# Kernel tuning notes

Measured on AMD Instinct MI355X. Metric: run time of the kernel, lower is better.

The kernel has to match this reference:

```python
import jax, jax.numpy as jnp
import numpy as np

S, B = 64, 16          # seq_len, batch
V = 32000              # ntoken
NINP = 512             # ninp (embedding / decoder input dim)
NHID = 1536            # nhid (intermediate LSTM layers)
NHL = 1024             # nhidlast (last LSTM layer)
E = 8                  # n_experts


def setup_inputs() -> dict:
    key = jax.random.key(0)
    ks = jax.random.split(key, 24)

    def unif(k, shape, r=0.1):
        return jax.random.uniform(k, shape, jnp.float32, -r, r)

    inp = {
        "tokens": jax.random.randint(ks[0], (S, B), 0, V),
        "h0": jnp.zeros((B, NHID), jnp.float32),
        "c0": jnp.zeros((B, NHID), jnp.float32),
        "h1": jnp.zeros((B, NHID), jnp.float32),
        "c1": jnp.zeros((B, NHID), jnp.float32),
        "h2": jnp.zeros((B, NHL), jnp.float32),
        "c2": jnp.zeros((B, NHL), jnp.float32),
        # parameters
        "emb": unif(ks[1], (V, NINP)),
        "Wih0": unif(ks[2], (4 * NHID, NINP)),
        "Whh0": unif(ks[3], (4 * NHID, NHID)),
        "b0": jnp.zeros((4 * NHID,), jnp.float32),
        "Wih1": unif(ks[4], (4 * NHID, NHID)),
        "Whh1": unif(ks[5], (4 * NHID, NHID)),
        "b1": jnp.zeros((4 * NHID,), jnp.float32),
        "Wih2": unif(ks[6], (4 * NHL, NHID)),
        "Whh2": unif(ks[7], (4 * NHL, NHL)),
        "b2": jnp.zeros((4 * NHL,), jnp.float32),
        "prior_W": unif(ks[8], (E, NHL)),
        "latent_W": unif(ks[9], (E * NINP, NHL)),
        "latent_b": jnp.zeros((E * NINP,), jnp.float32),
        "dec_W": unif(ks[10], (V, NINP)),
        "dec_b": jnp.zeros((V,), jnp.float32),
        "gain": jnp.ones((NINP,), jnp.float32),   # decoder_gain (frozen ones)
    }
    return inp


def _lstm_layer(x, h0, c0, Wih, Whh, b):
    # x: (S, B, Din); gate order i, f, g, o as in torch
    xg = jnp.einsum('sbd,gd->sbg', x, Wih) + b  # precompute input projections

    def step(carry, xt):
        h, c = carry
        g = xt + h @ Whh.T
        i, f, gg, o = jnp.split(g, 4, axis=-1)
        c = jax.nn.sigmoid(f) * c + jax.nn.sigmoid(i) * jnp.tanh(gg)
        h = jax.nn.sigmoid(o) * jnp.tanh(c)
        return (h, c), h

    (hT, cT), ys = jax.lax.scan(step, (h0, c0), xg)
    return ys, hT, cT


def reference(tokens, h0, c0, h1, c1, h2, c2, emb, Wih0, Whh0, b0,
              Wih1, Whh1, b1, Wih2, Whh2, b2, prior_W, latent_W, latent_b,
              dec_W, dec_b, gain):
    x = emb[tokens]                                   # (S, B, NINP)
    x, _, _ = _lstm_layer(x, h0, c0, Wih0, Whh0, b0)  # (S, B, NHID)
    x, _, _ = _lstm_layer(x, h1, c1, Wih1, Whh1, b1)  # (S, B, NHID)
    out, _, _ = _lstm_layer(x, h2, c2, Wih2, Whh2, b2)  # (S, B, NHL)

    # MoS head
    latent = jnp.tanh(jnp.einsum('sbh,eh->sbe', out, latent_W) + latent_b)
    latent = latent.reshape(S * B * E, NINP)          # (S*B*E, NINP)
    logit = (latent * gain) @ dec_W.T + dec_b         # (S*B*E, V)
    prior = jax.nn.softmax(out.reshape(S * B, NHL) @ prior_W.T, axis=-1)  # (S*B, E)
    prob = jax.nn.softmax(logit, axis=-1).reshape(S * B, E, V)
    prob = jnp.einsum('nev,ne->nv', prob, prior)      # mixture over experts
    log_prob = jnp.log(prob + 1e-8)
    return log_prob.reshape(S, B, V)
```

## Files before the change

### kernel.cpp

```cpp
#include <hip/hip_runtime.h>
#include <hip/hip_bf16.h>

typedef __attribute__((ext_vector_type(8))) short short8;
typedef __attribute__((ext_vector_type(4))) float f32x4;
typedef unsigned short u16;
typedef unsigned long long u64;

__device__ __forceinline__ u16 f2b(float f) {
    unsigned u = __float_as_uint(f);
    return (u16)((u + 0x7FFFu + ((u >> 16) & 1u)) >> 16);
}
__device__ __forceinline__ float b2f(u16 u) {
    return __uint_as_float(((unsigned)u) << 16);
}
__device__ __forceinline__ void gload16(const void* g, void* l) {
    __builtin_amdgcn_global_load_lds(
        (const __attribute__((address_space(1))) void*)g,
        (__attribute__((address_space(3))) void*)l, 16, 0, 0);
}

struct CvtJobs {
    const float* s[6];
    u16* d[6];
    int n4[6];
    int njobs;
};

__global__ __launch_bounds__(256)
void k_f2b(const float* __restrict__ s, u16* __restrict__ d, int n4)
{
    int i = blockIdx.x * 256 + threadIdx.x;
    if (i >= n4) return;
    float4 v = ((const float4*)s)[i];
    short4 o;
    o.x = (short)f2b(v.x); o.y = (short)f2b(v.y);
    o.z = (short)f2b(v.z); o.w = (short)f2b(v.w);
    ((short4*)d)[i] = o;
}

__global__ __launch_bounds__(256)
void k_embed(const int* __restrict__ tok, const float* __restrict__ emb,
             u16* __restrict__ x0)
{
    int i = blockIdx.x * 256 + threadIdx.x;
    int n = i >> 7, p4 = i & 127;
    float4 v = ((const float4*)(emb + (size_t)tok[n] * 512))[p4];
    short4 o;
    o.x = (short)f2b(v.x); o.y = (short)f2b(v.y);
    o.z = (short)f2b(v.z); o.w = (short)f2b(v.w);
    ((short4*)x0)[i] = o;
}

template <int EPI>
__global__ __launch_bounds__(256)
void k_gemm(const u16* __restrict__ A, const u16* __restrict__ B,
            const float* __restrict__ bias, void* __restrict__ Cp,
            int M, int N, int K, const float* __restrict__ gain,
            float* __restrict__ rsum)
{
    __shared__ __align__(16) u16 As[2][128 * 32];
    __shared__ __align__(16) u16 Bs[2][128 * 32];
    __shared__ float rs[2][128];
    const int tid = threadIdx.x;
    const int lane = tid & 63, wid = tid >> 6;
    const int wr = wid >> 1, wc = wid & 1;
    const int l15 = lane & 15, l4 = lane >> 4;
    const int row0 = blockIdx.y * 128, col0 = blockIdx.x * 128;

    const int srA = wid * 16 + (lane >> 2);
    const int skA = (lane & 3) * 8;

    auto stage = [&](int buf, int k0) {
        gload16(A + (size_t)(row0 + srA) * K + k0 + skA, &As[buf][wid * 512]);
        gload16(A + (size_t)(row0 + 64 + srA) * K + k0 + skA, &As[buf][2048 + wid * 512]);
        gload16(B + (size_t)(col0 + srA) * K + k0 + skA, &Bs[buf][wid * 512]);
        gload16(B + (size_t)(col0 + 64 + srA) * K + k0 + skA, &Bs[buf][2048 + wid * 512]);
    };

    f32x4 acc[4][4] = {};

    stage(0, 0);
    __syncthreads();
    int cur = 0;
    for (int k0 = 0; k0 < K; k0 += 32) {
        if (k0 + 32 < K) stage(cur ^ 1, k0 + 32);

        short8 af[4], bfv[4];
#pragma unroll
        for (int i = 0; i < 4; ++i)
            af[i]  = *(const short8*)&As[cur][(wr * 64 + i * 16 + l15) * 32 + l4 * 8];
#pragma unroll
        for (int i = 0; i < 4; ++i)
            bfv[i] = *(const short8*)&Bs[cur][(wc * 64 + i * 16 + l15) * 32 + l4 * 8];
#pragma unroll
        for (int mi = 0; mi < 4; ++mi)
#pragma unroll
            for (int ni = 0; ni < 4; ++ni)
                acc[mi][ni] = __builtin_amdgcn_mfma_f32_16x16x32_bf16(
                    af[mi], bfv[ni], acc[mi][ni], 0, 0, 0);
        __syncthreads();
        cur ^= 1;
    }

    if (EPI == 2) {
#pragma unroll
        for (int mi = 0; mi < 4; ++mi) {
#pragma unroll
            for (int j = 0; j < 4; ++j) {
                int rb = row0 + wr * 64 + mi * 16 + l4 * 4 + j;
                float rsub = 0.f;
#pragma unroll
                for (int ni = 0; ni < 4; ++ni) {
                    int cc = col0 + wc * 64 + ni * 16 + l15;
                    float pv = expf(fminf(acc[mi][ni][j] + bias[cc], 80.f));
                    ((u16*)Cp)[(size_t)rb * N + cc] = f2b(pv);
                    rsub += pv;
                }
#pragma unroll
                for (int o = 1; o < 16; o <<= 1) rsub += __shfl_xor(rsub, o, 64);
                if (l15 == 0)
                    rs[wc][wr * 64 + mi * 16 + l4 * 4 + j] = rsub;
            }
        }
        __syncthreads();
        if (tid < 128)
            atomicAdd(&rsum[row0 + tid], rs[0][tid] + rs[1][tid]);
        return;
    }

#pragma unroll
    for (int mi = 0; mi < 4; ++mi) {
#pragma unroll
        for (int ni = 0; ni < 4; ++ni) {
            int rb = row0 + wr * 64 + mi * 16 + l4 * 4;
            int cc = col0 + wc * 64 + ni * 16 + l15;
            float bv = bias[cc];
#pragma unroll
            for (int j = 0; j < 4; ++j) {
                float v = acc[mi][ni][j] + bv;
                if (EPI == 0) {
                    ((float*)Cp)[(size_t)(rb + j) * N + cc] = v;
                } else {
                    int e = cc >> 9, pp = cc & 511;
                    ((u16*)Cp)[(((size_t)(rb + j) * 8 + e) << 9) | pp] =
                        f2b(tanhf(v) * gain[pp]);
                }
            }
        }
    }
}

__global__ __launch_bounds__(512)
void k_gemm_dec(const u16* __restrict__ A, const u16* __restrict__ B,
                const float* __restrict__ bias, u16* __restrict__ pe,
                int M, int N, int K, float* __restrict__ rsum,
                const u16* __restrict__ pePrev, const float* __restrict__ prior,
                const float* __restrict__ rsumPrev, float* __restrict__ outp,
                int n0prev, int nPer)
{
    __shared__ __align__(16) u16 As[2][256 * 32];
    __shared__ __align__(16) u16 Bs[2][128 * 32];
    __shared__ float rs[2][256];
    const int tid = threadIdx.x;

    if ((int)blockIdx.y == (int)gridDim.y - 1) {
        if (n0prev < 0) return;
        float* wsh = (float*)As;
        for (int i = tid; i < nPer * 8; i += 512)
            wsh[i] = prior[(size_t)(n0prev + (i >> 3)) * 8 + (i & 7)]
                   / rsumPrev[i];
        __syncthreads();
        const int total = nPer * 32000;
        const int stride = gridDim.x * 512;
        for (int i = blockIdx.x * 512 + tid; i < total; i += stride) {
            int nl = i / 32000, v = i - nl * 32000;
            float acc = 0.f;
#pragma unroll
            for (int e = 0; e < 8; ++e)
                acc += b2f(pePrev[(size_t)(nl * 8 + e) * 32000 + v])
                     * wsh[nl * 8 + e];
            outp[(size_t)(n0prev + nl) * 32000 + v] = logf(acc + 1e-8f);
        }
        return;
    }

    const int lane = tid & 63, wid = tid >> 6;
    const int wr = wid >> 1, wc = wid & 1;
    const int l15 = lane & 15, l4 = lane >> 4;
    const int row0 = blockIdx.y * 256, col0 = blockIdx.x * 128;

    const int srA = wid * 16 + (lane >> 2);
    const int skA = (lane & 3) * 8;

    auto stage = [&](int buf, int k0) {
        gload16(A + (size_t)(row0 + srA) * K + k0 + skA, &As[buf][wid * 512]);
        gload16(A + (size_t)(row0 + 128 + srA) * K + k0 + skA, &As[buf][4096 + wid * 512]);
        gload16(B + (size_t)(col0 + srA) * K + k0 + skA, &Bs[buf][wid * 512]);
    };

    f32x4 acc[4][4] = {};

    stage(0, 0);
    __syncthreads();
    int cur = 0;
    for (int k0 = 0; k0 < K; k0 += 32) {
        if (k0 + 32 < K) stage(cur ^ 1, k0 + 32);

        short8 af[4], bfv[4];
#pragma unroll
        for (int i = 0; i < 4; ++i)
            af[i]  = *(const short8*)&As[cur][(wr * 64 + i * 16 + l15) * 32 + l4 * 8];
#pragma unroll
        for (int i = 0; i < 4; ++i)
            bfv[i] = *(const short8*)&Bs[cur][(wc * 64 + i * 16 + l15) * 32 + l4 * 8];
#pragma unroll
        for (int mi = 0; mi < 4; ++mi)
#pragma unroll
            for (int ni = 0; ni < 4; ++ni)
                acc[mi][ni] = __builtin_amdgcn_mfma_f32_16x16x32_bf16(
                    af[mi], bfv[ni], acc[mi][ni], 0, 0, 0);
        __syncthreads();
        cur ^= 1;
    }

#pragma unroll
    for (int mi = 0; mi < 4; ++mi) {
#pragma unroll
        for (int j = 0; j < 4; ++j) {
            int rloc = wr * 64 + mi * 16 + l4 * 4 + j;
            float rsub = 0.f;
#pragma unroll
            for (int ni = 0; ni < 4; ++ni) {
                int cc = col0 + wc * 64 + ni * 16 + l15;
                float pv = expf(fminf(acc[mi][ni][j] + bias[cc], 80.f));
                pe[(size_t)(row0 + rloc) * N + cc] = f2b(pv);
                rsub += pv;
            }
#pragma unroll
            for (int o = 1; o < 16; o <<= 1) rsub += __shfl_xor(rsub, o, 64);
            if (l15 == 0) rs[wc][rloc] = rsub;
        }
    }
    __syncthreads();
    if (tid < 256)
        atomicAdd(&rsum[row0 + tid], rs[0][tid] + rs[1][tid]);
}

template <int DH>
__global__ void __launch_bounds__(512)
k_rnn(const float* __restrict__ xg,
      const u16* __restrict__ W,
      const float* __restrict__ h0f,
      const float* __restrict__ c0f,
      u16* __restrict__ y,
      unsigned* __restrict__ bar,
      int nb, CvtJobs jobs)
{
    if ((int)blockIdx.x >= nb) {
        const int hb = blockIdx.x - nb, nh = gridDim.x - nb;
        for (int j = 0; j < jobs.njobs; ++j) {
            const float4* s = (const float4*)jobs.s[j];
            short4* d = (short4*)jobs.d[j];
            const int n4 = jobs.n4[j];
            for (int i = hb * 512 + threadIdx.x; i < n4; i += nh * 512) {
                float4 v = s[i];
                short4 o;
                o.x = (short)f2b(v.x); o.y = (short)f2b(v.y);
                o.z = (short)f2b(v.z); o.w = (short)f2b(v.w);
                d[i] = o;
            }
        }
        return;
    }

    constexpr int DH2 = DH / 2;
    constexpr int NSH = DH2 / 32;
    constexpr int NL  = 16 * DH / 4 / 512;
    constexpr int RW  = DH / 4;
    constexpr int LDH = DH + 8;
    __shared__ __align__(16) u16 hs[16][LDH];
    __shared__ __align__(16) f32x4 red[8][64];
    __shared__ __align__(16) u16 hout[16][16];

    const int tid = threadIdx.x;
    const int lane = tid & 63, wid = tid >> 6;
    const int g = wid & 3, kh = wid >> 2;
    const int l15 = lane & 15, l4 = lane >> 4;
    const int u0 = blockIdx.x * 16;

    short8 wfr[NSH];
    {
        const u16* wa = W + (size_t)(g * DH + u0 + l15) * DH + kh * DH2 + l4 * 8;
#pragma unroll
        for (int s = 0; s < NSH; ++s) wfr[s] = *(const short8*)(wa + s * 32);
    }

    const int eb = tid >> 4, eu = tid & 15;
    float c_reg = (tid < 256) ? c0f[(size_t)eb * DH + u0 + eu] : 0.f;

    for (int t = 0; t < 64; ++t) {
        float xpre[4];
        if (tid < 256) {
            const float* xr = xg + (size_t)(t * 16 + eb) * 4 * DH + u0 + eu;
#pragma unroll
            for (int gg = 0; gg < 4; ++gg) xpre[gg] = xr[(size_t)gg * DH];
        }

        if (t == 0) {
            for (int i = tid; i < 16 * DH / 4; i += 512) {
                int r = i / (DH / 4), k4 = i % (DH / 4);
                float4 v = *(const float4*)(h0f + (size_t)r * DH + k4 * 4);
                short4 o;
                o.x = (short)f2b(v.x); o.y = (short)f2b(v.y);
                o.z = (short)f2b(v.z); o.w = (short)f2b(v.w);
                *(short4*)&hs[r][k4 * 4] = o;
            }
            __syncthreads();
        } else {
            if (tid < nb) {
                while (__hip_atomic_load(bar + tid * 32, __ATOMIC_RELAXED,
                                         __HIP_MEMORY_SCOPE_AGENT) < (unsigned)t)
                    __builtin_amdgcn_s_sleep(1);
            }
            __syncthreads();
            const u64* hp = (const u64*)(y + (size_t)(t - 1) * 16 * DH);
            u64 tmp[NL];
#pragma unroll
            for (int j = 0; j < NL; ++j)
                tmp[j] = __hip_atomic_load(hp + tid + j * 512, __ATOMIC_RELAXED,
                                           __HIP_MEMORY_SCOPE_AGENT);
#pragma unroll
            for (int j = 0; j < NL; ++j) {
                int idx = tid + j * 512;
                int r = idx / RW, c = (idx % RW) * 4;
                *(u64*)&hs[r][c] = tmp[j];
            }
            __syncthreads();
        }

        f32x4 acc = {};
#pragma unroll
        for (int s = 0; s < NSH; ++s) {
            short8 hf = *(const short8*)&hs[l15][kh * DH2 + s * 32 + l4 * 8];
            acc = __builtin_amdgcn_mfma_f32_16x16x32_bf16(hf, wfr[s], acc, 0, 0, 0);
        }
        red[wid][lane] = acc;
        __syncthreads();

        if (tid < 256) {
            const int li = (eb >> 2) * 16 + eu, j = eb & 3;
            float gt[4];
#pragma unroll
            for (int gg = 0; gg < 4; ++gg)
                gt[gg] = ((const float*)&red[gg][li])[j]
                       + ((const float*)&red[4 + gg][li])[j]
                       + xpre[gg];
            float si = 1.f / (1.f + expf(-gt[0]));
            float sf = 1.f / (1.f + expf(-gt[1]));
            float so = 1.f / (1.f + expf(-gt[3]));
            c_reg = sf * c_reg + si * tanhf(gt[2]);
            hout[eb][eu] = f2b(so * tanhf(c_reg));
        }
        __syncthreads();

        if (tid < 64) {
            int r = tid >> 2, c4 = (tid & 3) * 4;
            u64 v = *(const u64*)&hout[r][c4];
            __hip_atomic_store((u64*)(y + (size_t)(t * 16 + r) * DH + u0 + c4), v,
                               __ATOMIC_RELAXED, __HIP_MEMORY_SCOPE_AGENT);
        }

        if (t < 63) {
            __syncthreads();
            if (tid == 0)
                __hip_atomic_store(bar + blockIdx.x * 32, (unsigned)(t + 1),
                                   __ATOMIC_RELAXED, __HIP_MEMORY_SCOPE_AGENT);
        }
    }
}

__global__ __launch_bounds__(256)
void k_prior(const u16* __restrict__ out2, const float* __restrict__ pW,
             float* __restrict__ prior)
{
    const int n = blockIdx.x;
    const int tid = threadIdx.x;
    const int e = tid >> 5, lane = tid & 31;
    const u16* x = out2 + (size_t)n * 1024;
    const float* w = pW + (size_t)e * 1024;
    float s = 0.f;
    for (int k = lane; k < 1024; k += 32) s += b2f(x[k]) * w[k];
#pragma unroll
    for (int o = 16; o; o >>= 1) s += __shfl_down(s, o, 32);
    __shared__ float es[8];
    if (lane == 0) es[e] = s;
    __syncthreads();
    if (tid == 0) {
        float m = -1e30f;
        for (int i = 0; i < 8; ++i) m = fmaxf(m, es[i]);
        float Z = 0.f, ex[8];
        for (int i = 0; i < 8; ++i) { ex[i] = expf(es[i] - m); Z += ex[i]; }
        for (int i = 0; i < 8; ++i) prior[(size_t)n * 8 + i] = ex[i] / Z;
    }
}

__global__ __launch_bounds__(128)
void k_combine(const u16* __restrict__ pe, const float* __restrict__ prior,
               const float* __restrict__ rsum, float* __restrict__ out, int n0)
{
    const int v2 = blockIdx.x * 128 + threadIdx.x;
    const int nl = blockIdx.y;
    __shared__ float w[8];
    if (threadIdx.x < 8)
        w[threadIdx.x] = prior[(size_t)(n0 + nl) * 8 + threadIdx.x]
                       / rsum[nl * 8 + threadIdx.x];
    __syncthreads();
    float a0 = 0.f, a1 = 0.f;
#pragma unroll
    for (int e = 0; e < 8; ++e) {
        unsigned pv = *(const unsigned*)&pe[(size_t)(nl * 8 + e) * 32000 + v2 * 2];
        a0 += b2f((u16)(pv & 0xffff)) * w[e];
        a1 += b2f((u16)(pv >> 16)) * w[e];
    }
    float2 o;
    o.x = logf(a0 + 1e-8f);
    o.y = logf(a1 + 1e-8f);
    *(float2*)&out[(size_t)(n0 + nl) * 32000 + v2 * 2] = o;
}

extern "C" void kernel_launch(void* const* d_in, const int* in_sizes, int n_in,
                              void* d_out, int out_size, void* d_ws, size_t ws_size,
                              hipStream_t stream)
{
    const int*   tok  = (const int*)d_in[0];
    const float* h0   = (const float*)d_in[1];
    const float* c0   = (const float*)d_in[2];
    const float* h1   = (const float*)d_in[3];
    const float* c1   = (const float*)d_in[4];
    const float* h2   = (const float*)d_in[5];
    const float* c2   = (const float*)d_in[6];
    const float* emb  = (const float*)d_in[7];
    const float* Wih0 = (const float*)d_in[8];
    const float* Whh0 = (const float*)d_in[9];
    const float* b0   = (const float*)d_in[10];
    const float* Wih1 = (const float*)d_in[11];
    const float* Whh1 = (const float*)d_in[12];
    const float* b1   = (const float*)d_in[13];
    const float* Wih2 = (const float*)d_in[14];
    const float* Whh2 = (const float*)d_in[15];
    const float* b2   = (const float*)d_in[16];
    const float* priW = (const float*)d_in[17];
    const float* latW = (const float*)d_in[18];
    const float* latb = (const float*)d_in[19];
    const float* decW = (const float*)d_in[20];
    const float* decb = (const float*)d_in[21];
    const float* gain = (const float*)d_in[22];

    char* p = (char*)d_ws;
    auto alloc = [&](size_t bytes) {
        char* r = p; p += (bytes + 255) & ~(size_t)255; return r;
    };
    u16* Whh0b = (u16*)alloc(6144ull * 1536 * 2);
    u16* Whh1b = (u16*)alloc(6144ull * 1536 * 2);
    u16* Whh2b = (u16*)alloc(4096ull * 1024 * 2);
    u16* latWb = (u16*)alloc(4096ull * 1024 * 2);
    u16* decWb = (u16*)alloc(32000ull * 512 * 2);
    u16* latb16 = (u16*)alloc(8192ull * 512 * 2);
    float* pri   = (float*)alloc(8192 * 4);
    float* rowsum = (float*)alloc(8192 * 4);
    u16* out2 = (u16*)alloc(1024ull * 1024 * 2);
    unsigned* bars = (unsigned*)alloc(3 * 96 * 32 * 4);
    char* trans = p;
    u16* Wih0b = (u16*)alloc(6144ull * 512 * 2);
    u16* Wih1b = (u16*)alloc(6144ull * 1536 * 2);
    u16* Wih2b = (u16*)alloc(4096ull * 1536 * 2);
    u16* x0 = (u16*)alloc(1024ull * 512 * 2);
    u16* x1 = (u16*)alloc(1024ull * 1536 * 2);
    u16* x2 = (u16*)alloc(1024ull * 1536 * 2);
    float* xg = (float*)alloc(1024ull * 6144 * 4);
    size_t cap = ws_size - (size_t)(trans - (char*)d_ws);
    int chunkRows;
    bool fused;
    if      (cap >= 2ull * 1024 * 32000 * 2) { chunkRows = 1024; fused = true; }
    else if (cap >= 2ull * 512 * 32000 * 2)  { chunkRows = 512;  fused = true; }
    else if (cap >= 2ull * 256 * 32000 * 2)  { chunkRows = 256;  fused = true; }
    else                                     { chunkRows = 128;  fused = false; }
    int nPer = chunkRows / 8;
    size_t chunkElems = (size_t)chunkRows * 32000;
    u16* pe0 = (u16*)trans;
    u16* pe1 = pe0 + chunkElems;

    hipMemsetAsync(bars, 0, 3 * 96 * 32 * 4, stream);
    hipMemsetAsync(rowsum, 0, 8192 * 4, stream);

    k_f2b<<<9216, 256, 0, stream>>>(Whh0, Whh0b, 2359296);
    k_f2b<<<3072, 256, 0, stream>>>(Wih0, Wih0b, 786432);
    k_embed<<<512, 256, 0, stream>>>(tok, emb, x0);

    k_gemm<0><<<dim3(48, 8), 256, 0, stream>>>(
        x0, Wih0b, b0, xg, 1024, 6144, 512, nullptr, nullptr);
    {
        unsigned* bar = bars;
        int nb = 96;
        CvtJobs jobs;
        jobs.s[0] = Whh1; jobs.d[0] = Whh1b; jobs.n4[0] = 2359296;
        jobs.s[1] = Whh2; jobs.d[1] = Whh2b; jobs.n4[1] = 1048576;
        jobs.s[2] = Wih1; jobs.d[2] = Wih1b; jobs.n4[2] = 2359296;
        jobs.s[3] = Wih2; jobs.d[3] = Wih2b; jobs.n4[3] = 1572864;
        jobs.s[4] = latW; jobs.d[4] = latWb; jobs.n4[4] = 1048576;
        jobs.s[5] = decW; jobs.d[5] = decWb; jobs.n4[5] = 4096000;
        jobs.njobs = 6;
        void* args[] = {(void*)&xg, (void*)&Whh0b, (void*)&h0, (void*)&c0,
                        (void*)&x1, (void*)&bar, (void*)&nb, (void*)&jobs};
        hipLaunchCooperativeKernel(reinterpret_cast<void*>(&k_rnn<1536>),
                                   dim3(256), dim3(512), args, 0, stream);
    }

    k_gemm<0><<<dim3(48, 8), 256, 0, stream>>>(
        x1, Wih1b, b1, xg, 1024, 6144, 1536, nullptr, nullptr);
    {
        unsigned* bar = bars + 96 * 32;
        int nb = 96;
        CvtJobs jobs;
        jobs.njobs = 0;
        void* args[] = {(void*)&xg, (void*)&Whh1b, (void*)&h1, (void*)&c1,
                        (void*)&x2, (void*)&bar, (void*)&nb, (void*)&jobs};
        hipLaunchCooperativeKernel(reinterpret_cast<void*>(&k_rnn<1536>),
                                   dim3(96), dim3(512), args, 0, stream);
    }

    k_gemm<0><<<dim3(32, 8), 256, 0, stream>>>(
        x2, Wih2b, b2, xg, 1024, 4096, 1536, nullptr, nullptr);
    {
        unsigned* bar = bars + 2 * 96 * 32;
        int nb = 64;
        CvtJobs jobs;
        jobs.njobs = 0;
        void* args[] = {(void*)&xg, (void*)&Whh2b, (void*)&h2, (void*)&c2,
                        (void*)&out2, (void*)&bar, (void*)&nb, (void*)&jobs};
        hipLaunchCooperativeKernel(reinterpret_cast<void*>(&k_rnn<1024>),
                                   dim3(64), dim3(512), args, 0, stream);
    }

    k_prior<<<1024, 256, 0, stream>>>(out2, priW, pri);
    k_gemm<1><<<dim3(32, 8), 256, 0, stream>>>(
        out2, latWb, latb, latb16, 1024, 4096, 1024, gain, nullptr);

    if (fused) {
        const int rowTiles = chunkRows / 256;
        const int nChunks = 1024 / nPer;
        for (int ci = 0; ci < nChunks; ++ci) {
            int nb = ci * nPer;
            u16* peCur = (ci & 1) ? pe1 : pe0;
            const u16* pePrev = (ci & 1) ? pe0 : pe1;
            int n0prev = nb - nPer;
            const float* rsPrev = rowsum + (size_t)(n0prev < 0 ? 0 : n0prev) * 8;
            k_gemm_dec<<<dim3(250, rowTiles + 1), 512, 0, stream>>>(
                latb16 + (size_t)nb * 8 * 512, decWb, decb, peCur,
                chunkRows, 32000, 512, rowsum + (size_t)nb * 8,
                pePrev, pri, rsPrev, (float*)d_out, n0prev, nPer);
        }
        int n0t = 1024 - nPer;
        const u16* peLast = ((nChunks - 1) & 1) ? pe1 : pe0;
        k_combine<<<dim3(125, nPer), 128, 0, stream>>>(
            peLast, pri, rowsum + (size_t)n0t * 8, (float*)d_out, n0t);
    } else {
        for (int nb = 0; nb < 1024; nb += nPer) {
            const u16* Ach = latb16 + (size_t)nb * 8 * 512;
            float* rsumc = rowsum + (size_t)nb * 8;
            k_gemm<2><<<dim3(250, chunkRows / 128), 256, 0, stream>>>(
                Ach, decWb, decb, pe0, chunkRows, 32000, 512, nullptr, rsumc);
            k_combine<<<dim3(125, nPer), 128, 0, stream>>>(
                pe0, pri, rsumc, (float*)d_out, nb);
        }
    }
}
```

Measured before the change: 1.424 ms.

## Replace per-step flag barrier with sentinel-polled hidden state in recurrent kernel

Drops the per-block step-counter barrier in the persistent LSTM kernel. Output buffers are now pre-filled with 0xFF, and each thread polls its own 8-byte chunk of the previous hidden state until it no longer holds the all-ones sentinel. This removes one barrier round trip per timestep, both the flag store and the polling load, and lets threads proceed as soon as their data arrives. The cost is three extra memsets, plus a reliance on no valid bf16 quad ever equalling the all-ones pattern (a NaN pattern) and on the 8-byte stores being atomic.

```diff
diff --git a/kernel.cpp b/kernel.cpp
--- a/kernel.cpp
+++ b/kernel.cpp
@@ -5,6 +5,8 @@
 typedef __attribute__((ext_vector_type(4))) float f32x4;
 typedef unsigned short u16;
 typedef unsigned long long u64;
+
+#define SENT 0xFFFFFFFFFFFFFFFFull
 
 __device__ __forceinline__ u16 f2b(float f) {
     unsigned u = __float_as_uint(f);
@@ -253,7 +255,6 @@
       const float* __restrict__ h0f,
       const float* __restrict__ c0f,
       u16* __restrict__ y,
-      unsigned* __restrict__ bar,
       int nb, CvtJobs jobs)
 {
     if ((int)blockIdx.x >= nb) {
@@ -317,18 +318,25 @@
             }
             __syncthreads();
         } else {
-            if (tid < nb) {
-                while (__hip_atomic_load(bar + tid * 32, __ATOMIC_RELAXED,
-                                         __HIP_MEMORY_SCOPE_AGENT) < (unsigned)t)
-                    __builtin_amdgcn_s_sleep(1);
-            }
-            __syncthreads();
             const u64* hp = (const u64*)(y + (size_t)(t - 1) * 16 * DH);
             u64 tmp[NL];
 #pragma unroll
             for (int j = 0; j < NL; ++j)
                 tmp[j] = __hip_atomic_load(hp + tid + j * 512, __ATOMIC_RELAXED,
                                            __HIP_MEMORY_SCOPE_AGENT);
+            for (;;) {
+                bool done = true;
+#pragma unroll
+                for (int j = 0; j < NL; ++j) done &= (tmp[j] != SENT);
+                if (done) break;
+                __builtin_amdgcn_s_sleep(1);
+#pragma unroll
+                for (int j = 0; j < NL; ++j)
+                    if (tmp[j] == SENT)
+                        tmp[j] = __hip_atomic_load(hp + tid + j * 512,
+                                                   __ATOMIC_RELAXED,
+                                                   __HIP_MEMORY_SCOPE_AGENT);
+            }
 #pragma unroll
             for (int j = 0; j < NL; ++j) {
                 int idx = tid + j * 512;
@@ -369,13 +377,7 @@
             __hip_atomic_store((u64*)(y + (size_t)(t * 16 + r) * DH + u0 + c4), v,
                                __ATOMIC_RELAXED, __HIP_MEMORY_SCOPE_AGENT);
         }
-
-        if (t < 63) {
-            __syncthreads();
-            if (tid == 0)
-                __hip_atomic_store(bar + blockIdx.x * 32, (unsigned)(t + 1),
-                                   __ATOMIC_RELAXED, __HIP_MEMORY_SCOPE_AGENT);
-        }
+        if (t < 63) __syncthreads();
     }
 }
 
@@ -469,7 +471,6 @@
     float* pri   = (float*)alloc(8192 * 4);
     float* rowsum = (float*)alloc(8192 * 4);
     u16* out2 = (u16*)alloc(1024ull * 1024 * 2);
-    unsigned* bars = (unsigned*)alloc(3 * 96 * 32 * 4);
     char* trans = p;
     u16* Wih0b = (u16*)alloc(6144ull * 512 * 2);
     u16* Wih1b = (u16*)alloc(6144ull * 1536 * 2);
@@ -490,8 +491,10 @@
     u16* pe0 = (u16*)trans;
     u16* pe1 = pe0 + chunkElems;
 
-    hipMemsetAsync(bars, 0, 3 * 96 * 32 * 4, stream);
     hipMemsetAsync(rowsum, 0, 8192 * 4, stream);
+    hipMemsetAsync(x1, 0xFF, 1024ull * 1536 * 2, stream);
+    hipMemsetAsync(x2, 0xFF, 1024ull * 1536 * 2, stream);
+    hipMemsetAsync(out2, 0xFF, 1024ull * 1024 * 2, stream);
 
     k_f2b<<<9216, 256, 0, stream>>>(Whh0, Whh0b, 2359296);
     k_f2b<<<3072, 256, 0, stream>>>(Wih0, Wih0b, 786432);
@@ -500,7 +503,6 @@
     k_gemm<0><<<dim3(48, 8), 256, 0, stream>>>(
         x0, Wih0b, b0, xg, 1024, 6144, 512, nullptr, nullptr);
     {
-        unsigned* bar = bars;
         int nb = 96;
         CvtJobs jobs;
         jobs.s[0] = Whh1; jobs.d[0] = Whh1b; jobs.n4[0] = 2359296;
@@ -511,7 +513,7 @@
         jobs.s[5] = decW; jobs.d[5] = decWb; jobs.n4[5] = 4096000;
         jobs.njobs = 6;
         void* args[] = {(void*)&xg, (void*)&Whh0b, (void*)&h0, (void*)&c0,
-                        (void*)&x1, (void*)&bar, (void*)&nb, (void*)&jobs};
+                        (void*)&x1, (void*)&nb, (void*)&jobs};
         hipLaunchCooperativeKernel(reinterpret_cast<void*>(&k_rnn<1536>),
                                    dim3(256), dim3(512), args, 0, stream);
     }
@@ -519,12 +521,11 @@
     k_gemm<0><<<dim3(48, 8), 256, 0, stream>>>(
         x1, Wih1b, b1, xg, 1024, 6144, 1536, nullptr, nullptr);
     {
-        unsigned* bar = bars + 96 * 32;
         int nb = 96;
         CvtJobs jobs;
         jobs.njobs = 0;
         void* args[] = {(void*)&xg, (void*)&Whh1b, (void*)&h1, (void*)&c1,
-                        (void*)&x2, (void*)&bar, (void*)&nb, (void*)&jobs};
+                        (void*)&x2, (void*)&nb, (void*)&jobs};
         hipLaunchCooperativeKernel(reinterpret_cast<void*>(&k_rnn<1536>),
                                    dim3(96), dim3(512), args, 0, stream);
     }
@@ -532,12 +533,11 @@
     k_gemm<0><<<dim3(32, 8), 256, 0, stream>>>(
         x2, Wih2b, b2, xg, 1024, 4096, 1536, nullptr, nullptr);
     {
-        unsigned* bar = bars + 2 * 96 * 32;
         int nb = 64;
         CvtJobs jobs;
         jobs.njobs = 0;
         void* args[] = {(void*)&xg, (void*)&Whh2b, (void*)&h2, (void*)&c2,
-                        (void*)&out2, (void*)&bar, (void*)&nb, (void*)&jobs};
+                        (void*)&out2, (void*)&nb, (void*)&jobs};
         hipLaunchCooperativeKernel(reinterpret_cast<void*>(&k_rnn<1024>),
                                    dim3(64), dim3(512), args, 0, stream);
     }
```

After: 1.494 ms. 1.05x slower.

## Overlap next layer's input projection with recurrent steps via helper blocks

Applied to the files above, without the earlier changes.

Spare blocks in the cooperative RNN launch now compute the next LSTM layer's input-projection GEMM, reading fp32 weights and converting them on the fly. They poll per-block step flags, and each 128-row tile starts once its 8 timesteps of hidden output are published. This removes the separate Wih1/Wih2 conversions and the standalone projection GEMMs between layers. Double-buffered xg arrays (xgA/xgB) make this possible. In exchange, helper blocks compete with the latency-critical recurrent blocks for bandwidth, and they rely on relaxed atomics and spin-waiting, so visibility of the published hidden states depends on those flags.

```diff
diff --git a/kernel.cpp b/kernel.cpp
--- a/kernel.cpp
+++ b/kernel.cpp
@@ -19,11 +19,15 @@
         (__attribute__((address_space(3))) void*)l, 16, 0, 0);
 }
 
-struct CvtJobs {
-    const float* s[6];
-    u16* d[6];
-    int n4[6];
-    int njobs;
+struct HelperWork {
+    const float* cs[4]; u16* cd[4]; int cn4[4]; int ncvt;
+    const u16* ysrc;
+    const float* Wf;
+    const float* bias;
+    float* xgOut;
+    int K, NC4;
+    unsigned* flags; int nflags;
+    int doproj;
 };
 
 __global__ __launch_bounds__(256)
@@ -246,6 +250,81 @@
         atomicAdd(&rsum[row0 + tid], rs[0][tid] + rs[1][tid]);
 }
 
+__device__ void helper_proj(u16* lds, const HelperWork& hw, int hb, int nh)
+{
+    u16* As = lds;
+    u16* Bs = lds + 4096;
+    const int tid = threadIdx.x;
+    const int lane = tid & 63, wid = tid >> 6;
+    const int wr = wid >> 2, wc = wid & 3;
+    const int l15 = lane & 15, l4 = lane >> 4;
+    const int K = hw.K, NC4 = hw.NC4;
+    const int NC = NC4 >> 7, NT = 8 * NC;
+
+    for (int idx = hb; idx < NT; idx += nh) {
+        const int rg = idx / NC, ct = idx - rg * NC;
+        const int row0 = rg * 128, col0 = ct * 128;
+        if (tid < hw.nflags) {
+            const unsigned tgt = 8u * rg + 8u;
+            while (__hip_atomic_load(hw.flags + tid * 32, __ATOMIC_RELAXED,
+                                     __HIP_MEMORY_SCOPE_AGENT) < tgt)
+                __builtin_amdgcn_s_sleep(1);
+        }
+        __syncthreads();
+
+        f32x4 acc[4][2] = {};
+        for (int k0 = 0; k0 < K; k0 += 32) {
+#pragma unroll
+            for (int it = 0; it < 2; ++it) {
+                int i = tid + it * 512;
+                int r = i >> 3, c8 = i & 7;
+                u64 v = __hip_atomic_load(
+                    (const u64*)(hw.ysrc + (size_t)(row0 + r) * K + k0 + c8 * 4),
+                    __ATOMIC_RELAXED, __HIP_MEMORY_SCOPE_AGENT);
+                *(u64*)&As[r * 32 + c8 * 4] = v;
+            }
+            {
+                int srow = tid >> 2, q = tid & 3;
+                const float4* src =
+                    (const float4*)(hw.Wf + (size_t)(col0 + srow) * K + k0 + q * 8);
+                float4 v0 = src[0], v1 = src[1];
+                short8 o;
+                o[0] = (short)f2b(v0.x); o[1] = (short)f2b(v0.y);
+                o[2] = (short)f2b(v0.z); o[3] = (short)f2b(v0.w);
+                o[4] = (short)f2b(v1.x); o[5] = (short)f2b(v1.y);
+                o[6] = (short)f2b(v1.z); o[7] = (short)f2b(v1.w);
+                *(short8*)&Bs[srow * 32 + q * 8] = o;
+            }
+            __syncthreads();
+            short8 af[4], bfv[2];
+#pragma unroll
+            for (int i = 0; i < 4; ++i)
+                af[i] = *(const short8*)&As[(wr * 64 + i * 16 + l15) * 32 + l4 * 8];
+#pragma unroll
+            for (int i = 0; i < 2; ++i)
+                bfv[i] = *(const short8*)&Bs[(wc * 32 + i * 16 + l15) * 32 + l4 * 8];
+#pragma unroll
+            for (int mi = 0; mi < 4; ++mi)
+#pragma unroll
+                for (int ni = 0; ni < 2; ++ni)
+                    acc[mi][ni] = __builtin_amdgcn_mfma_f32_16x16x32_bf16(
+                        af[mi], bfv[ni], acc[mi][ni], 0, 0, 0);
+            __syncthreads();
+        }
+#pragma unroll
+        for (int mi = 0; mi < 4; ++mi)
+#pragma unroll
+            for (int ni = 0; ni < 2; ++ni) {
+                int rb = row0 + wr * 64 + mi * 16 + l4 * 4;
+                int cc = col0 + wc * 32 + ni * 16 + l15;
+                float bv = hw.bias[cc];
+#pragma unroll
+                for (int j = 0; j < 4; ++j)
+                    hw.xgOut[(size_t)(rb + j) * NC4 + cc] = acc[mi][ni][j] + bv;
+            }
+    }
+}
+
 template <int DH>
 __global__ void __launch_bounds__(512)
 k_rnn(const float* __restrict__ xg,
@@ -254,25 +333,8 @@
       const float* __restrict__ c0f,
       u16* __restrict__ y,
       unsigned* __restrict__ bar,
-      int nb, CvtJobs jobs)
-{
-    if ((int)blockIdx.x >= nb) {
-        const int hb = blockIdx.x - nb, nh = gridDim.x - nb;
-        for (int j = 0; j < jobs.njobs; ++j) {
-            const float4* s = (const float4*)jobs.s[j];
-            short4* d = (short4*)jobs.d[j];
-            const int n4 = jobs.n4[j];
-            for (int i = hb * 512 + threadIdx.x; i < n4; i += nh * 512) {
-                float4 v = s[i];
-                short4 o;
-                o.x = (short)f2b(v.x); o.y = (short)f2b(v.y);
-                o.z = (short)f2b(v.z); o.w = (short)f2b(v.w);
-                d[i] = o;
-            }
-        }
-        return;
-    }
-
+      int nb, HelperWork hw)
+{
     constexpr int DH2 = DH / 2;
     constexpr int NSH = DH2 / 32;
     constexpr int NL  = 16 * DH / 4 / 512;
@@ -283,6 +345,25 @@
     __shared__ __align__(16) u16 hout[16][16];
 
     const int tid = threadIdx.x;
+
+    if ((int)blockIdx.x >= nb) {
+        const int hb = blockIdx.x - nb, nh = gridDim.x - nb;
+        for (int j = 0; j < hw.ncvt; ++j) {
+            const float4* s = (const float4*)hw.cs[j];
+            short4* d = (short4*)hw.cd[j];
+            const int n4 = hw.cn4[j];
+            for (int i = hb * 512 + tid; i < n4; i += nh * 512) {
+                float4 v = s[i];
+                short4 o;
+                o.x = (short)f2b(v.x); o.y = (short)f2b(v.y);
+                o.z = (short)f2b(v.z); o.w = (short)f2b(v.w);
+                d[i] = o;
+            }
+        }
+        if (hw.doproj) helper_proj(&hs[0][0], hw, hb, nh);
+        return;
+    }
+
     const int lane = tid & 63, wid = tid >> 6;
     const int g = wid & 3, kh = wid >> 2;
     const int l15 = lane & 15, l4 = lane >> 4;
@@ -370,12 +451,10 @@
                                __ATOMIC_RELAXED, __HIP_MEMORY_SCOPE_AGENT);
         }
 
-        if (t < 63) {
-            __syncthreads();
-            if (tid == 0)
-                __hip_atomic_store(bar + blockIdx.x * 32, (unsigned)(t + 1),
-                                   __ATOMIC_RELAXED, __HIP_MEMORY_SCOPE_AGENT);
-        }
+        __syncthreads();
+        if (tid == 0)
+            __hip_atomic_store(bar + blockIdx.x * 32, (unsigned)(t + 1),
+                               __ATOMIC_RELAXED, __HIP_MEMORY_SCOPE_AGENT);
     }
 }
 
@@ -472,12 +551,11 @@
     unsigned* bars = (unsigned*)alloc(3 * 96 * 32 * 4);
     char* trans = p;
     u16* Wih0b = (u16*)alloc(6144ull * 512 * 2);
-    u16* Wih1b = (u16*)alloc(6144ull * 1536 * 2);
-    u16* Wih2b = (u16*)alloc(4096ull * 1536 * 2);
     u16* x0 = (u16*)alloc(1024ull * 512 * 2);
     u16* x1 = (u16*)alloc(1024ull * 1536 * 2);
     u16* x2 = (u16*)alloc(1024ull * 1536 * 2);
-    float* xg = (float*)alloc(1024ull * 6144 * 4);
+    float* xgA = (float*)alloc(1024ull * 6144 * 4);
+    float* xgB = (float*)alloc(1024ull * 6144 * 4);
     size_t cap = ws_size - (size_t)(trans - (char*)d_ws);
     int chunkRows;
     bool fused;
@@ -498,46 +576,47 @@
     k_embed<<<512, 256, 0, stream>>>(tok, emb, x0);
 
     k_gemm<0><<<dim3(48, 8), 256, 0, stream>>>(
-        x0, Wih0b, b0, xg, 1024, 6144, 512, nullptr, nullptr);
+        x0, Wih0b, b0, xgA, 1024, 6144, 512, nullptr, nullptr);
+
     {
         unsigned* bar = bars;
         int nb = 96;
-        CvtJobs jobs;
-        jobs.s[0] = Whh1; jobs.d[0] = Whh1b; jobs.n4[0] = 2359296;
-        jobs.s[1] = Whh2; jobs.d[1] = Whh2b; jobs.n4[1] = 1048576;
-        jobs.s[2] = Wih1; jobs.d[2] = Wih1b; jobs.n4[2] = 2359296;
-        jobs.s[3] = Wih2; jobs.d[3] = Wih2b; jobs.n4[3] = 1572864;
-        jobs.s[4] = latW; jobs.d[4] = latWb; jobs.n4[4] = 1048576;
-        jobs.s[5] = decW; jobs.d[5] = decWb; jobs.n4[5] = 4096000;
-        jobs.njobs = 6;
-        void* args[] = {(void*)&xg, (void*)&Whh0b, (void*)&h0, (void*)&c0,
-                        (void*)&x1, (void*)&bar, (void*)&nb, (void*)&jobs};
+        HelperWork hw;
+        hw.cs[0] = Whh1; hw.cd[0] = Whh1b; hw.cn4[0] = 2359296;
+        hw.cs[1] = Whh2; hw.cd[1] = Whh2b; hw.cn4[1] = 1048576;
+        hw.cs[2] = latW; hw.cd[2] = latWb; hw.cn4[2] = 1048576;
+        hw.cs[3] = decW; hw.cd[3] = decWb; hw.cn4[3] = 4096000;
+        hw.ncvt = 4;
+        hw.ysrc = x1; hw.Wf = Wih1; hw.bias = b1; hw.xgOut = xgB;
+        hw.K = 1536; hw.NC4 = 6144;
+        hw.flags = bars; hw.nflags = 96; hw.doproj = 1;
+        void* args[] = {(void*)&xgA, (void*)&Whh0b, (void*)&h0, (void*)&c0,
+                        (void*)&x1, (void*)&bar, (void*)&nb, (void*)&hw};
         hipLaunchCooperativeKernel(reinterpret_cast<void*>(&k_rnn<1536>),
                                    dim3(256), dim3(512), args, 0, stream);
     }
 
-    k_gemm<0><<<dim3(48, 8), 256, 0, stream>>>(
-        x1, Wih1b, b1, xg, 1024, 6144, 1536, nullptr, nullptr);
     {
         unsigned* bar = bars + 96 * 32;
         int nb = 96;
-        CvtJobs jobs;
-        jobs.njobs = 0;
-        void* args[] = {(void*)&xg, (void*)&Whh1b, (void*)&h1, (void*)&c1,
-                        (void*)&x2, (void*)&bar, (void*)&nb, (void*)&jobs};
+        HelperWork hw;
+        hw.ncvt = 0;
+        hw.ysrc = x2; hw.Wf = Wih2; hw.bias = b2; hw.xgOut = xgA;
+        hw.K = 1536; hw.NC4 = 4096;
+        hw.flags = bars + 96 * 32; hw.nflags = 96; hw.doproj = 1;
+        void* args[] = {(void*)&xgB, (void*)&Whh1b, (void*)&h1, (void*)&c1,
+                        (void*)&x2, (void*)&bar, (void*)&nb, (void*)&hw};
         hipLaunchCooperativeKernel(reinterpret_cast<void*>(&k_rnn<1536>),
-                                   dim3(96), dim3(512), args, 0, stream);
-    }
-
-    k_gemm<0><<<dim3(32, 8), 256, 0, stream>>>(
-        x2, Wih2b, b2, xg, 1024, 4096, 1536, nullptr, nullptr);
+                                   dim3(256), dim3(512), args, 0, stream);
+    }
+
     {
         unsigned* bar = bars + 2 * 96 * 32;
         int nb = 64;
-        CvtJobs jobs;
-        jobs.njobs = 0;
-        void* args[] = {(void*)&xg, (void*)&Whh2b, (void*)&h2, (void*)&c2,
-                        (void*)&out2, (void*)&bar, (void*)&nb, (void*)&jobs};
+        HelperWork hw;
+        hw.ncvt = 0; hw.doproj = 0;
+        void* args[] = {(void*)&xgA, (void*)&Whh2b, (void*)&h2, (void*)&c2,
+                        (void*)&out2, (void*)&bar, (void*)&nb, (void*)&hw};
         hipLaunchCooperativeKernel(reinterpret_cast<void*>(&k_rnn<1024>),
                                    dim3(64), dim3(512), args, 0, stream);
     }
```

Result: slower. 1.466 ms (+3.0%).

## Fuse weight conversion and prior into GEMMs, remap decoder tiles by XCD

Applied to the files above, without the earlier changes.

The first input-projection GEMM now reads fp32 Wih0 directly and converts it to bf16 while staging into LDS. An extra row of blocks converts Whh0 in parallel, which removes two standalone conversion launches and the Wih0b buffer. The prior softmax is folded into extra blocks of the latent GEMM, so k_prior is no longer a separate launch. The decoder GEMM block indices are remapped so that consecutive work items land on the same XCD for better L2 locality. The cost is per-tile conversion work inside the first GEMM and a serialized 32-row loop in the prior helper blocks.

```diff
diff --git a/kernel.cpp b/kernel.cpp
--- a/kernel.cpp
+++ b/kernel.cpp
@@ -25,18 +25,6 @@
     int n4[6];
     int njobs;
 };
-
-__global__ __launch_bounds__(256)
-void k_f2b(const float* __restrict__ s, u16* __restrict__ d, int n4)
-{
-    int i = blockIdx.x * 256 + threadIdx.x;
-    if (i >= n4) return;
-    float4 v = ((const float4*)s)[i];
-    short4 o;
-    o.x = (short)f2b(v.x); o.y = (short)f2b(v.y);
-    o.z = (short)f2b(v.z); o.w = (short)f2b(v.w);
-    ((short4*)d)[i] = o;
-}
 
 __global__ __launch_bounds__(256)
 void k_embed(const int* __restrict__ tok, const float* __restrict__ emb,
@@ -51,17 +39,58 @@
     ((short4*)x0)[i] = o;
 }
 
-template <int EPI>
+template <int EPI, int BIN, int HELP>
 __global__ __launch_bounds__(256)
-void k_gemm(const u16* __restrict__ A, const u16* __restrict__ B,
+void k_gemm(const u16* __restrict__ A, const void* __restrict__ Bp,
             const float* __restrict__ bias, void* __restrict__ Cp,
             int M, int N, int K, const float* __restrict__ gain,
-            float* __restrict__ rsum)
+            float* __restrict__ rsum,
+            const float* __restrict__ xs, void* __restrict__ xd, int xn)
 {
     __shared__ __align__(16) u16 As[2][128 * 32];
     __shared__ __align__(16) u16 Bs[2][128 * 32];
     __shared__ float rs[2][128];
     const int tid = threadIdx.x;
+
+    if (HELP == 1 && (int)blockIdx.y == (int)gridDim.y - 1) {
+        const float4* s = (const float4*)xs;
+        short4* d = (short4*)xd;
+        for (int i = blockIdx.x * 256 + tid; i < xn; i += gridDim.x * 256) {
+            float4 v = s[i];
+            short4 o;
+            o.x = (short)f2b(v.x); o.y = (short)f2b(v.y);
+            o.z = (short)f2b(v.z); o.w = (short)f2b(v.w);
+            d[i] = o;
+        }
+        return;
+    }
+    if (HELP == 2 && (int)blockIdx.y == (int)gridDim.y - 1) {
+        const float* pW = xs;
+        float* pri = (float*)xd;
+        const int e = tid >> 5, lane = tid & 31;
+        float* es = rs[0];
+        for (int ni = 0; ni < 32; ++ni) {
+            int n = blockIdx.x * 32 + ni;
+            const u16* x = A + (size_t)n * 1024;
+            const float* w = pW + (size_t)e * 1024;
+            float s = 0.f;
+            for (int k = lane; k < 1024; k += 32) s += b2f(x[k]) * w[k];
+#pragma unroll
+            for (int o = 16; o; o >>= 1) s += __shfl_down(s, o, 32);
+            if (lane == 0) es[e] = s;
+            __syncthreads();
+            if (tid == 0) {
+                float m = -1e30f;
+                for (int i = 0; i < 8; ++i) m = fmaxf(m, es[i]);
+                float Z = 0.f, ex[8];
+                for (int i = 0; i < 8; ++i) { ex[i] = expf(es[i] - m); Z += ex[i]; }
+                for (int i = 0; i < 8; ++i) pri[(size_t)n * 8 + i] = ex[i] / Z;
+            }
+            __syncthreads();
+        }
+        return;
+    }
+
     const int lane = tid & 63, wid = tid >> 6;
     const int wr = wid >> 1, wc = wid & 1;
     const int l15 = lane & 15, l4 = lane >> 4;
@@ -69,12 +98,31 @@
 
     const int srA = wid * 16 + (lane >> 2);
     const int skA = (lane & 3) * 8;
+    const int srow = tid >> 1, skh = (tid & 1) << 4;
 
     auto stage = [&](int buf, int k0) {
         gload16(A + (size_t)(row0 + srA) * K + k0 + skA, &As[buf][wid * 512]);
         gload16(A + (size_t)(row0 + 64 + srA) * K + k0 + skA, &As[buf][2048 + wid * 512]);
-        gload16(B + (size_t)(col0 + srA) * K + k0 + skA, &Bs[buf][wid * 512]);
-        gload16(B + (size_t)(col0 + 64 + srA) * K + k0 + skA, &Bs[buf][2048 + wid * 512]);
+        if (BIN == 1) {
+            const u16* B = (const u16*)Bp;
+            gload16(B + (size_t)(col0 + srA) * K + k0 + skA, &Bs[buf][wid * 512]);
+            gload16(B + (size_t)(col0 + 64 + srA) * K + k0 + skA, &Bs[buf][2048 + wid * 512]);
+        } else {
+            const float* Bf = (const float*)Bp;
+            const float4* sb = (const float4*)(Bf + (size_t)(col0 + srow) * K + k0 + skh);
+            float4 v0 = sb[0], v1 = sb[1], v2 = sb[2], v3 = sb[3];
+            short8 o0, o1;
+            o0[0] = (short)f2b(v0.x); o0[1] = (short)f2b(v0.y);
+            o0[2] = (short)f2b(v0.z); o0[3] = (short)f2b(v0.w);
+            o0[4] = (short)f2b(v1.x); o0[5] = (short)f2b(v1.y);
+            o0[6] = (short)f2b(v1.z); o0[7] = (short)f2b(v1.w);
+            o1[0] = (short)f2b(v2.x); o1[1] = (short)f2b(v2.y);
+            o1[2] = (short)f2b(v2.z); o1[3] = (short)f2b(v2.w);
+            o1[4] = (short)f2b(v3.x); o1[5] = (short)f2b(v3.y);
+            o1[6] = (short)f2b(v3.z); o1[7] = (short)f2b(v3.w);
+            *(short8*)&Bs[buf][srow * 32 + skh]     = o0;
+            *(short8*)&Bs[buf][srow * 32 + skh + 8] = o1;
+        }
     };
 
     f32x4 acc[4][4] = {};
@@ -163,16 +211,25 @@
     __shared__ float rs[2][256];
     const int tid = threadIdx.x;
 
-    if ((int)blockIdx.y == (int)gridDim.y - 1) {
+    const int gx = gridDim.x, gy = gridDim.y;
+    const int total = gx * gy;
+    const int f = (int)blockIdx.y * gx + (int)blockIdx.x;
+    const int q = total >> 3, r = total & 7;
+    const int xcd = f & 7, idx = f >> 3;
+    const int work = (xcd < r) ? xcd * (q + 1) + idx
+                               : r * (q + 1) + (xcd - r) * q + idx;
+    const int wx = work / gy, wy = work - wx * gy;
+
+    if (wy == gy - 1) {
         if (n0prev < 0) return;
         float* wsh = (float*)As;
         for (int i = tid; i < nPer * 8; i += 512)
             wsh[i] = prior[(size_t)(n0prev + (i >> 3)) * 8 + (i & 7)]
                    / rsumPrev[i];
         __syncthreads();
-        const int total = nPer * 32000;
-        const int stride = gridDim.x * 512;
-        for (int i = blockIdx.x * 512 + tid; i < total; i += stride) {
+        const int total2 = nPer * 32000;
+        const int stride = gx * 512;
+        for (int i = wx * 512 + tid; i < total2; i += stride) {
             int nl = i / 32000, v = i - nl * 32000;
             float acc = 0.f;
 #pragma unroll
@@ -187,7 +244,7 @@
     const int lane = tid & 63, wid = tid >> 6;
     const int wr = wid >> 1, wc = wid & 1;
     const int l15 = lane & 15, l4 = lane >> 4;
-    const int row0 = blockIdx.y * 256, col0 = blockIdx.x * 128;
+    const int row0 = wy * 256, col0 = wx * 128;
 
     const int srA = wid * 16 + (lane >> 2);
     const int skA = (lane & 3) * 8;
@@ -376,31 +433,6 @@
                 __hip_atomic_store(bar + blockIdx.x * 32, (unsigned)(t + 1),
                                    __ATOMIC_RELAXED, __HIP_MEMORY_SCOPE_AGENT);
         }
-    }
-}
-
-__global__ __launch_bounds__(256)
-void k_prior(const u16* __restrict__ out2, const float* __restrict__ pW,
-             float* __restrict__ prior)
-{
-    const int n = blockIdx.x;
-    const int tid = threadIdx.x;
-    const int e = tid >> 5, lane = tid & 31;
-    const u16* x = out2 + (size_t)n * 1024;
-    const float* w = pW + (size_t)e * 1024;
-    float s = 0.f;
-    for (int k = lane; k < 1024; k += 32) s += b2f(x[k]) * w[k];
-#pragma unroll
-    for (int o = 16; o; o >>= 1) s += __shfl_down(s, o, 32);
-    __shared__ float es[8];
-    if (lane == 0) es[e] = s;
-    __syncthreads();
-    if (tid == 0) {
-        float m = -1e30f;
-        for (int i = 0; i < 8; ++i) m = fmaxf(m, es[i]);
-        float Z = 0.f, ex[8];
-        for (int i = 0; i < 8; ++i) { ex[i] = expf(es[i] - m); Z += ex[i]; }
-        for (int i = 0; i < 8; ++i) prior[(size_t)n * 8 + i] = ex[i] / Z;
     }
 }
 
@@ -471,7 +503,6 @@
     u16* out2 = (u16*)alloc(1024ull * 1024 * 2);
     unsigned* bars = (unsigned*)alloc(3 * 96 * 32 * 4);
     char* trans = p;
-    u16* Wih0b = (u16*)alloc(6144ull * 512 * 2);
     u16* Wih1b = (u16*)alloc(6144ull * 1536 * 2);
     u16* Wih2b = (u16*)alloc(4096ull * 1536 * 2);
     u16* x0 = (u16*)alloc(1024ull * 512 * 2);
@@ -493,12 +524,11 @@
     hipMemsetAsync(bars, 0, 3 * 96 * 32 * 4, stream);
     hipMemsetAsync(rowsum, 0, 8192 * 4, stream);
 
-    k_f2b<<<9216, 256, 0, stream>>>(Whh0, Whh0b, 2359296);
-    k_f2b<<<3072, 256, 0, stream>>>(Wih0, Wih0b, 786432);
     k_embed<<<512, 256, 0, stream>>>(tok, emb, x0);
-
-    k_gemm<0><<<dim3(48, 8), 256, 0, stream>>>(
-        x0, Wih0b, b0, xg, 1024, 6144, 512, nullptr, nullptr);
+    k_gemm<0, 0, 1><<<dim3(48, 9), 256, 0, stream>>>(
+        x0, Wih0, b0, xg, 1024, 6144, 512, nullptr, nullptr,
+        Whh0, Whh0b, 2359296);
+
     {
         unsigned* bar = bars;
         int nb = 96;
@@ -516,8 +546,9 @@
                                    dim3(256), dim3(512), args, 0, stream);
     }
 
-    k_gemm<0><<<dim3(48, 8), 256, 0, stream>>>(
-        x1, Wih1b, b1, xg, 1024, 6144, 1536, nullptr, nullptr);
+    k_gemm<0, 1, 0><<<dim3(48, 8), 256, 0, stream>>>(
+        x1, Wih1b, b1, xg, 1024, 6144, 1536, nullptr, nullptr,
+        nullptr, nullptr, 0);
     {
         unsigned* bar = bars + 96 * 32;
         int nb = 96;
@@ -529,8 +560,9 @@
                                    dim3(96), dim3(512), args, 0, stream);
     }
 
-    k_gemm<0><<<dim3(32, 8), 256, 0, stream>>>(
-        x2, Wih2b, b2, xg, 1024, 4096, 1536, nullptr, nullptr);
+    k_gemm<0, 1, 0><<<dim3(32, 8), 256, 0, stream>>>(
+        x2, Wih2b, b2, xg, 1024, 4096, 1536, nullptr, nullptr,
+        nullptr, nullptr, 0);
     {
         unsigned* bar = bars + 2 * 96 * 32;
         int nb = 64;
@@ -542,9 +574,9 @@
                                    dim3(64), dim3(512), args, 0, stream);
     }
 
-    k_prior<<<1024, 256, 0, stream>>>(out2, priW, pri);
-    k_gemm<1><<<dim3(32, 8), 256, 0, stream>>>(
-        out2, latWb, latb, latb16, 1024, 4096, 1024, gain, nullptr);
+    k_gemm<1, 1, 2><<<dim3(32, 9), 256, 0, stream>>>(
+        out2, latWb, latb, latb16, 1024, 4096, 1024, gain, nullptr,
+        priW, pri, 0);
 
     if (fused) {
         const int rowTiles = chunkRows / 256;
@@ -568,8 +600,9 @@
         for (int nb = 0; nb < 1024; nb += nPer) {
             const u16* Ach = latb16 + (size_t)nb * 8 * 512;
             float* rsumc = rowsum + (size_t)nb * 8;
-            k_gemm<2><<<dim3(250, chunkRows / 128), 256, 0, stream>>>(
-                Ach, decWb, decb, pe0, chunkRows, 32000, 512, nullptr, rsumc);
+            k_gemm<2, 1, 0><<<dim3(250, chunkRows / 128), 256, 0, stream>>>(
+                Ach, decWb, decb, pe0, chunkRows, 32000, 512, nullptr, rsumc,
+                nullptr, nullptr, 0);
             k_combine<<<dim3(125, nPer), 128, 0, stream>>>(
                 pe0, pri, rsumc, (float*)d_out, nb);
         }
```

Measured after the change: 1.547 ms. +8.7%, slower.
